# Optimization experiments

Measured on AMD Instinct MI355X. Metric: run time of the kernel, lower is better.

Reference implementation:

```python
import jax, jax.numpy as jnp
import numpy as np

BIG_NEG = 1e10  # mask fill value used by the original wlsep


def setup_inputs() -> dict:
    key = jax.random.key(0)
    k1, k2 = jax.random.split(key)
    B, C = 4096, 128
    output = jax.random.normal(k1, (B, C), dtype=jnp.float32)
    target = jax.random.randint(k2, (B, C), 0, 2, dtype=jnp.int32)
    return {"output": output, "target": target}


def reference(output, target):
    x = output.astype(jnp.float32)          # [B, C] logits
    labels = target.astype(jnp.float32)     # [B, C] {0,1}

    # ---- bce: -mean over all elements of log(sig) if target!=0 else log(1-sig)
    # log(sigmoid(x)) = log_sigmoid(x); log(1 - sigmoid(x)) = log_sigmoid(-x)
    log_p = jax.nn.log_sigmoid(x)
    log_1mp = jax.nn.log_sigmoid(-x)
    bce_loss = -jnp.mean(jnp.where(labels == 0, log_1mp, log_p))

    # ---- wlsep ----
    # mask[b,i,j] = labels[b,j] > labels[b,i]  (j positive, i negative)
    mask = (labels[:, None, :] > labels[:, :, None]).astype(jnp.float32)  # [B,C,C]
    # diffs[b,i,j] = scores[b,i] - scores[b,j]
    diffs = x[:, :, None] - x[:, None, :]                                  # [B,C,C]
    masked = diffs - (1.0 - mask) * BIG_NEG
    # F.pad(pad=(0,0,0,1)) appends a zero row along dim=1, then logsumexp over dim=1
    B, C = x.shape
    padded = jnp.concatenate([masked, jnp.zeros((B, 1, C), dtype=masked.dtype)], axis=1)
    lse = jax.nn.logsumexp(padded, axis=1)  # [B, C]
    pos = labels > 0
    wlsep_loss = jnp.sum(jnp.where(pos, lse, 0.0)) / jnp.sum(pos)

    return bce_loss + wlsep_loss
```

## Files before the change

kernel.cpp:

```cpp
#include <hip/hip_runtime.h>
#include <math.h>


#define C_DIM 128
#define RPW   4
#define TPB   256

typedef unsigned int u32;
typedef unsigned long long u64;

__device__ __forceinline__ float neg_log_sigmoid(float z) {
    return fmaxf(-z, 0.0f) + log1pf(__expf(-fabsf(z)));
}

__device__ __forceinline__ u64 pack_checked(float f) {
    u32 v = __float_as_uint(f);
    return (u64)v | ((u64)(~v) << 32);
}

__global__ __launch_bounds__(TPB) void bce_wlsep_onepass(
        const float* __restrict__ x, const int* __restrict__ t,
        u64* __restrict__ slots,
        float* __restrict__ out, int B, int nblocks, float inv_BC) {
    const int wave = threadIdx.x >> 6;
    const int lane = threadIdx.x & 63;
    const int row0 = (blockIdx.x * 4 + wave) * RPW;

    float2 xs[RPW]; int2 ts[RPW];
    #pragma unroll
    for (int k = 0; k < RPW; ++k) {
        const int r = row0 + k;
        if (r < B) {
            xs[k] = ((const float2*)(x + (size_t)r * C_DIM))[lane];
            ts[k] = ((const int2*)(t + (size_t)r * C_DIM))[lane];
        } else { xs[k] = make_float2(0.f, 0.f); ts[k] = make_int2(1, 1); }
    }

    float bce = 0.f, wl = 0.f, pos = 0.f;
    #pragma unroll
    for (int k = 0; k < RPW; ++k) {
        if (row0 + k >= B) break;
        const float x0 = xs[k].x, x1 = xs[k].y;
        const int   t0 = ts[k].x,  t1 = ts[k].y;

        bce += neg_log_sigmoid(t0 ? x0 : -x0) + neg_log_sigmoid(t1 ? x1 : -x1);

        float m = -INFINITY;
        if (!t0) m = x0;
        if (!t1) m = fmaxf(m, x1);
        #pragma unroll
        for (int off = 32; off; off >>= 1) m = fmaxf(m, __shfl_xor(m, off, 64));

        float T = 0.f;
        if (!t0) T += __expf(x0 - m);
        if (!t1) T += __expf(x1 - m);
        #pragma unroll
        for (int off = 32; off; off >>= 1) T += __shfl_xor(T, off, 64);

        if (t0) {
            float a = m - x0;
            wl += (a > 0.f) ? a + __logf(T + __expf(-a)) : log1pf(T * __expf(a));
            pos += 1.f;
        }
        if (t1) {
            float a = m - x1;
            wl += (a > 0.f) ? a + __logf(T + __expf(-a)) : log1pf(T * __expf(a));
            pos += 1.f;
        }
    }

    #pragma unroll
    for (int off = 32; off; off >>= 1) {
        bce += __shfl_xor(bce, off, 64);
        wl  += __shfl_xor(wl,  off, 64);
        pos += __shfl_xor(pos, off, 64);
    }
    __shared__ float s[3][4];
    if (lane == 0) { s[0][wave] = bce; s[1][wave] = wl; s[2][wave] = pos; }
    __syncthreads();
    if (threadIdx.x == 0) {
        float b = s[0][0] + s[0][1] + s[0][2] + s[0][3];
        float w = s[1][0] + s[1][1] + s[1][2] + s[1][3];
        float p = s[2][0] + s[2][1] + s[2][2] + s[2][3];
        __hip_atomic_store(&slots[3*blockIdx.x+0], pack_checked(b), __ATOMIC_RELAXED, __HIP_MEMORY_SCOPE_AGENT);
        __hip_atomic_store(&slots[3*blockIdx.x+1], pack_checked(w), __ATOMIC_RELAXED, __HIP_MEMORY_SCOPE_AGENT);
        __hip_atomic_store(&slots[3*blockIdx.x+2], pack_checked(p), __ATOMIC_RELAXED, __HIP_MEMORY_SCOPE_AGENT);
    }

    if (blockIdx.x != (unsigned)(nblocks - 1)) return;

    float fb = 0.f, fw = 0.f, fp = 0.f;
    for (int i = threadIdx.x; i < nblocks; i += TPB) {
        u64 v;
        do { v = __hip_atomic_load(&slots[3*i+0], __ATOMIC_RELAXED, __HIP_MEMORY_SCOPE_AGENT); }
        while ((u32)(v >> 32) != ~(u32)v);
        fb += __uint_as_float((u32)v);
        do { v = __hip_atomic_load(&slots[3*i+1], __ATOMIC_RELAXED, __HIP_MEMORY_SCOPE_AGENT); }
        while ((u32)(v >> 32) != ~(u32)v);
        fw += __uint_as_float((u32)v);
        do { v = __hip_atomic_load(&slots[3*i+2], __ATOMIC_RELAXED, __HIP_MEMORY_SCOPE_AGENT); }
        while ((u32)(v >> 32) != ~(u32)v);
        fp += __uint_as_float((u32)v);
    }
    #pragma unroll
    for (int off = 32; off; off >>= 1) {
        fb += __shfl_xor(fb, off, 64);
        fw += __shfl_xor(fw, off, 64);
        fp += __shfl_xor(fp, off, 64);
    }
    __syncthreads();
    if (lane == 0) { s[0][wave] = fb; s[1][wave] = fw; s[2][wave] = fp; }
    __syncthreads();
    if (threadIdx.x == 0) {
        float b = s[0][0] + s[0][1] + s[0][2] + s[0][3];
        float w = s[1][0] + s[1][1] + s[1][2] + s[1][3];
        float p = s[2][0] + s[2][1] + s[2][2] + s[2][3];
        out[0] = b * inv_BC + w / p;
    }
}

extern "C" void kernel_launch(void* const* d_in, const int* in_sizes, int n_in,
                              void* d_out, int out_size, void* d_ws, size_t ws_size,
                              hipStream_t stream) {
    const float* x = (const float*)d_in[0];
    const int*   t = (const int*)d_in[1];
    float* out = (float*)d_out;
    u64* slots = (u64*)d_ws;

    const int total = in_sizes[0];
    const int B = total / C_DIM;
    const int blocks = (B + RPW * 4 - 1) / (RPW * 4);

    bce_wlsep_onepass<<<blocks, TPB, 0, stream>>>(x, t, slots, out,
                                                  B, blocks, 1.0f / (float)total);
}
```

Baseline: 62.61 us.

## Split each wave into half-waves per row with float4 loads and simplified lse

Each wave now processes two rows at once, one per 32-lane half, loading float4/int4 per lane instead of float2/int2. This halves the number of sequential row iterations and shortens the shuffle reductions to five steps. The per-positive logsumexp is rewritten as softplus(L - x) with L = m + log(T), and log1pf is replaced with __logf(1+exp) to cut transcendental cost. The fast log form may lose some precision for large arguments, and T can be zero in a row with no negatives, which relies on inf handling.

```diff
diff --git a/kernel.cpp b/kernel.cpp
--- a/kernel.cpp
+++ b/kernel.cpp
@@ -3,14 +3,13 @@
 
 
 #define C_DIM 128
-#define RPW   4
 #define TPB   256
 
 typedef unsigned int u32;
 typedef unsigned long long u64;
 
-__device__ __forceinline__ float neg_log_sigmoid(float z) {
-    return fmaxf(-z, 0.0f) + log1pf(__expf(-fabsf(z)));
+__device__ __forceinline__ float softplus_fast(float z) {
+    return fmaxf(z, 0.0f) + __logf(1.0f + __expf(-fabsf(z)));
 }
 
 __device__ __forceinline__ u64 pack_checked(float f) {
@@ -24,48 +23,52 @@
         float* __restrict__ out, int B, int nblocks, float inv_BC) {
     const int wave = threadIdx.x >> 6;
     const int lane = threadIdx.x & 63;
-    const int row0 = (blockIdx.x * 4 + wave) * RPW;
+    const int half = lane >> 5;
+    const int sub  = lane & 31;
+    const int base = (blockIdx.x * 4 + wave) * 4;
 
-    float2 xs[RPW]; int2 ts[RPW];
+    const float4* xq = (const float4*)x;
+    const int4*   tq = (const int4*)t;
+
+    float4 xv[2]; int4 tv[2];
     #pragma unroll
-    for (int k = 0; k < RPW; ++k) {
-        const int r = row0 + k;
+    for (int it = 0; it < 2; ++it) {
+        const int r = base + 2 * it + half;
         if (r < B) {
-            xs[k] = ((const float2*)(x + (size_t)r * C_DIM))[lane];
-            ts[k] = ((const int2*)(t + (size_t)r * C_DIM))[lane];
-        } else { xs[k] = make_float2(0.f, 0.f); ts[k] = make_int2(1, 1); }
+            xv[it] = xq[(size_t)r * (C_DIM / 4) + sub];
+            tv[it] = tq[(size_t)r * (C_DIM / 4) + sub];
+        } else {
+            xv[it] = make_float4(-INFINITY, -INFINITY, -INFINITY, -INFINITY);
+            tv[it] = make_int4(0, 0, 0, 0);
+        }
     }
 
     float bce = 0.f, wl = 0.f, pos = 0.f;
     #pragma unroll
-    for (int k = 0; k < RPW; ++k) {
-        if (row0 + k >= B) break;
-        const float x0 = xs[k].x, x1 = xs[k].y;
-        const int   t0 = ts[k].x,  t1 = ts[k].y;
-
-        bce += neg_log_sigmoid(t0 ? x0 : -x0) + neg_log_sigmoid(t1 ? x1 : -x1);
+    for (int it = 0; it < 2; ++it) {
+        const float xe[4] = {xv[it].x, xv[it].y, xv[it].z, xv[it].w};
+        const int   te[4] = {tv[it].x, tv[it].y, tv[it].z, tv[it].w};
 
         float m = -INFINITY;
-        if (!t0) m = x0;
-        if (!t1) m = fmaxf(m, x1);
         #pragma unroll
-        for (int off = 32; off; off >>= 1) m = fmaxf(m, __shfl_xor(m, off, 64));
+        for (int e = 0; e < 4; ++e) {
+            bce += softplus_fast(te[e] ? -xe[e] : xe[e]);
+            if (!te[e]) m = fmaxf(m, xe[e]);
+        }
+        #pragma unroll
+        for (int off = 16; off; off >>= 1) m = fmaxf(m, __shfl_xor(m, off, 64));
 
         float T = 0.f;
-        if (!t0) T += __expf(x0 - m);
-        if (!t1) T += __expf(x1 - m);
         #pragma unroll
-        for (int off = 32; off; off >>= 1) T += __shfl_xor(T, off, 64);
+        for (int e = 0; e < 4; ++e)
+            if (!te[e]) T += __expf(xe[e] - m);
+        #pragma unroll
+        for (int off = 16; off; off >>= 1) T += __shfl_xor(T, off, 64);
 
-        if (t0) {
-            float a = m - x0;
-            wl += (a > 0.f) ? a + __logf(T + __expf(-a)) : log1pf(T * __expf(a));
-            pos += 1.f;
-        }
-        if (t1) {
-            float a = m - x1;
-            wl += (a > 0.f) ? a + __logf(T + __expf(-a)) : log1pf(T * __expf(a));
-            pos += 1.f;
+        const float L = m + __logf(T);
+        #pragma unroll
+        for (int e = 0; e < 4; ++e) {
+            if (te[e]) { wl += softplus_fast(L - xe[e]); pos += 1.f; }
         }
     }
 
@@ -75,6 +78,7 @@
         wl  += __shfl_xor(wl,  off, 64);
         pos += __shfl_xor(pos, off, 64);
     }
+
     __shared__ float s[3][4];
     if (lane == 0) { s[0][wave] = bce; s[1][wave] = wl; s[2][wave] = pos; }
     __syncthreads();
@@ -129,7 +133,7 @@
 
     const int total = in_sizes[0];
     const int B = total / C_DIM;
-    const int blocks = (B + RPW * 4 - 1) / (RPW * 4);
+    const int blocks = (B + 15) / 16;
 
     bce_wlsep_onepass<<<blocks, TPB, 0, stream>>>(x, t, slots, out,
                                                   B, blocks, 1.0f / (float)total);
```

After: 58.91 us (median of 2 runs). -5.9%, faster.
